# Optimization experiments

Measured on AMD Instinct MI355X. Metric: run time of the kernel, lower is better.

Reference implementation:

```python
import jax, jax.numpy as jnp
import numpy as np

H = 16  # n_heads (init kwarg)


def pos_enc(length, dim):
    # torch PositionalEncoding: pe[:,0::2]=sin, pe[:,1::2]=cos
    pos = jnp.arange(length, dtype=jnp.float32)[:, None]
    div = jnp.exp(jnp.arange(0, dim, 2, dtype=jnp.float32) * (-np.log(10000.0) / dim))
    ang = pos * div  # [L, dim/2]
    return jnp.stack([jnp.sin(ang), jnp.cos(ang)], axis=-1).reshape(length, dim)


def torch_ln(x, a, b, eps=1e-6):
    # custom LayerNorm: a*(x-mean)/(std+eps)+b with unbiased std (torch default)
    mean = x.mean(-1, keepdims=True)
    n = x.shape[-1]
    var = ((x - mean) ** 2).sum(-1, keepdims=True) / (n - 1)
    return a * (x - mean) / (jnp.sqrt(var) + eps) + b


def setup_inputs() -> dict:
    key = jax.random.key(0)
    ks = jax.random.split(key, 16)
    B, Lq, Lk, qd, kd, hid, mid = 8, 512, 1024, 768, 768, 1024, 4096
    s = 0.02  # weight init scale
    w = lambda k, shape: jax.random.normal(k, shape, jnp.float32) * s
    return dict(
        q=jax.random.normal(ks[0], (B, Lq, qd), jnp.float32),
        k=jax.random.normal(ks[1], (B, Lk, kd), jnp.float32),
        Wq=w(ks[2], (qd, hid)), bq=jnp.zeros(hid, jnp.float32),
        Wk=w(ks[3], (kd, hid)), bk=jnp.zeros(hid, jnp.float32),
        Wv=w(ks[4], (kd, hid)), bv=jnp.zeros(hid, jnp.float32),
        Wv0=w(ks[5], (kd, hid)), bv0=jnp.zeros(hid, jnp.float32),
        Wq0=w(ks[6], (qd, hid)), bq0=jnp.zeros(hid, jnp.float32),
        nq_a=jnp.ones(hid, jnp.float32), nq_b=jnp.zeros(hid, jnp.float32),
        nx_a=jnp.ones(hid, jnp.float32), nx_b=jnp.zeros(hid, jnp.float32),
        W1=w(ks[7], (hid, mid)), b1=jnp.zeros(mid, jnp.float32),
        W2=w(ks[8], (mid, hid)), b2=jnp.zeros(hid, jnp.float32),
        ns_a=jnp.ones(hid, jnp.float32), ns_b=jnp.zeros(hid, jnp.float32),
    )


def reference(q, k, Wq, bq, Wk, bk, Wv, bv, Wv0, bv0, Wq0, bq0,
              nq_a, nq_b, nx_a, nx_b, W1, b1, W2, b2, ns_a, ns_b):
    # FocalAtt(mode='CA').forward(q, k, PE='qk', SF=True, outmode='atted_bilinear')
    B, Lq, qd = q.shape
    Lk, kd = k.shape[1], k.shape[2]
    hid = Wq.shape[1]
    dh = hid // H
    q0 = q
    qp = q + pos_enc(Lq, qd)  # PosEnc_q (dropout=0)
    kp = k + pos_enc(Lk, kd)  # PosEnc_k
    # AttM: manual multi-head scores
    qh = (qp @ Wq + bq).reshape(B, Lq, H, dh).transpose(0, 2, 1, 3)  # bhqd
    kh = (kp @ Wk + bk).reshape(B, Lk, H, dh).transpose(0, 2, 1, 3)  # bhkd
    scores = jnp.einsum('bhqd,bhkd->bhqk', qh, kh) / jnp.sqrt(jnp.float32(dh))
    att = jax.nn.softmax(scores, axis=-1)  # SF=True
    q0p = q0 @ Wq0 + bq0  # [B, Lq, hid]
    # 'atted' branch
    v1 = (kp @ Wv + bv).reshape(B, Lk, H, dh).transpose(0, 2, 1, 3)
    atted = jnp.einsum('bhqk,bhkd->bhqd', att, v1)
    atted = atted.transpose(0, 2, 1, 3).reshape(B, Lq, hid)
    atted = torch_ln(q0p + atted, nq_a, nq_b)
    # 'bilinear' branch: einsum('bhvk,bhvq,bhqk->bhk')
    q0h = q0p.reshape(B, Lq, H, dh).transpose(0, 2, 1, 3)  # bhvd, v=Lq
    v0 = (kp @ Wv0 + bv0).reshape(B, Lk, H, dh).transpose(0, 2, 1, 3)  # bhqd, q=Lk
    x = jnp.einsum('bhvd,bhvq,bhqd->bhd', q0h, att, v0).reshape(B, hid)
    x = torch_ln(x, nx_a, nx_b)
    # attention output: relu over scores, mean over heads
    att_out = jax.nn.relu(scores).sum(axis=1) / jnp.float32(H)  # [B, Lq, Lk]
    # SorCA: FFN + residual + LayerNorm
    ff = jax.nn.relu(atted @ W1 + b1) @ W2 + b2
    qq = torch_ln(atted + ff, ns_a, ns_b)
    # FocalAtt returns (feature, q, k, attention, attidx_q, attidx_k); drop Nones
    return (x, qq, kp, att_out)
```

## Files before the change

kernel.cpp:

```cpp
#include <hip/hip_runtime.h>


typedef unsigned short bfr;
using short8 = __attribute__((ext_vector_type(8))) short;
using f32x4  = __attribute__((ext_vector_type(4))) float;

__device__ __forceinline__ float b2f(bfr s) {
  return __uint_as_float(((unsigned int)s) << 16);
}
__device__ __forceinline__ bfr f2b(float f) {
  unsigned int u = __float_as_uint(f);
  u += 0x7fffu + ((u >> 16) & 1u);
  return (bfr)(u >> 16);
}

struct __align__(8) us4 { bfr x, y, z, w; };

__device__ __forceinline__ float4 load4f(const float* p) { return *(const float4*)p; }
__device__ __forceinline__ float4 load4f(const bfr* p) {
  us4 u = *(const us4*)p;
  return make_float4(b2f(u.x), b2f(u.y), b2f(u.z), b2f(u.w));
}
__device__ __forceinline__ void store4(float* p, float a, float b, float c, float d) {
  *(float4*)p = make_float4(a, b, c, d);
}
__device__ __forceinline__ void store4(bfr* p, float a, float b, float c, float d) {
  us4 v; v.x = f2b(a); v.y = f2b(b); v.z = f2b(c); v.w = f2b(d);
  *(us4*)p = v;
}

__device__ __forceinline__ void gll16(const bfr* g, bfr* l) {
  __builtin_amdgcn_global_load_lds(
      (const __attribute__((address_space(1))) unsigned int*)g,
      (__attribute__((address_space(3))) unsigned int*)l, 16, 0, 0);
}

__device__ __forceinline__ int swz_off(int row, int chunk) {
  return row * 64 + ((chunk ^ (row & 7)) * 8);
}

__device__ __forceinline__ float pe_val(int l, int d) {
  float ang = (float)l * expf((float)(d & ~1) * (-9.210340371976184f / 768.0f));
  return (d & 1) ? cosf(ang) : sinf(ang);
}

__global__ __launch_bounds__(256) void posenc_k(const float* __restrict__ in,
                                                float* __restrict__ outf,
                                                bfr* __restrict__ outb, int total) {
  int idx = blockIdx.x * 256 + threadIdx.x;
  if (idx >= total) return;
  float v = in[idx] + pe_val((idx / 768) % 1024, idx % 768);
  outf[idx] = v;
  outb[idx] = f2b(v);
}

__global__ __launch_bounds__(256) void posenc_q_all(const float* __restrict__ in,
                                                    bfr* __restrict__ out,
                                                    bfr* __restrict__ outraw,
                                                    int total) {
  int idx = blockIdx.x * 256 + threadIdx.x;
  if (idx >= total) return;
  float v = in[idx];
  out[idx] = f2b(v + pe_val((idx / 768) % 512, idx % 768));
  outraw[idx] = f2b(v);
}

__global__ __launch_bounds__(256) void transpose_w(const float* __restrict__ src,
                                                   bfr* __restrict__ dst,
                                                   int rows, int cols, int ld,
                                                   int mode) {
  __shared__ float t[32][33];
  const int bc = blockIdx.x * 32, br = blockIdx.y * 32;
  const int tx = threadIdx.x & 31, ty = threadIdx.x >> 5;
#pragma unroll
  for (int i = 0; i < 4; i++)
    t[ty + i * 8][tx] = src[(size_t)(br + ty + i * 8) * ld + bc + tx];
  __syncthreads();
#pragma unroll
  for (int i = 0; i < 4; i++) {
    int c = bc + ty + i * 8;
    int r = (mode == 0) ? c : ((c >> 6) * 128 + (c & 63) + (mode == 2 ? 64 : 0));
    dst[(size_t)r * rows + br + tx] = f2b(t[tx][ty + i * 8]);
  }
}

template <typename TC>
__device__ __forceinline__ void mgemm_body64(const bfr* __restrict__ A,
                                             const bfr* __restrict__ BT,
                                             const float* __restrict__ bias,
                                             TC* __restrict__ C,
                                             int K, int ldc, int relu, int accum,
                                             int m0, int n0,
                                             bfr* __restrict__ As,
                                             bfr* __restrict__ Bs) {
  const int tid = threadIdx.x;
  const int lane = tid & 63, w = tid >> 6;
  const int wm = (w & 1) * 64, wn = (w >> 1) * 32;
  const int grow = lane >> 3;
  const int gkc = ((lane & 7) ^ (lane >> 3)) * 8;
  const int fr = lane & 15, fcg = lane >> 4;
  const int NT = K >> 6;
  f32x4 acc[4][2];
#pragma unroll
  for (int i = 0; i < 4; i++)
#pragma unroll
    for (int j = 0; j < 2; j++) acc[i][j] = (f32x4){0.f, 0.f, 0.f, 0.f};

  auto issue = [&](int t, int buf) {
    const int k0 = t << 6;
    const bfr* Ag = A + (size_t)(m0 + w * 32 + grow) * K + k0 + gkc;
#pragma unroll
    for (int i = 0; i < 4; i++)
      gll16(Ag + (size_t)(i * 8) * K, As + buf * 8192 + (w * 32 + i * 8) * 64);
    const bfr* Bg = BT + (size_t)(n0 + w * 16 + grow) * K + k0 + gkc;
#pragma unroll
    for (int i = 0; i < 2; i++)
      gll16(Bg + (size_t)(i * 8) * K, Bs + buf * 4096 + (w * 16 + i * 8) * 64);
  };

  issue(0, 0);
  asm volatile("s_waitcnt vmcnt(0)" ::: "memory");
  __builtin_amdgcn_s_barrier();
  __builtin_amdgcn_sched_barrier(0);
  int cur = 0;
  for (int t = 0; t < NT; ++t) {
    const bool more = (t + 1 < NT);
    if (more) issue(t + 1, cur ^ 1);
    __builtin_amdgcn_s_setprio(1);
#pragma unroll
    for (int ks = 0; ks < 2; ks++) {
      short8 af[4], bf4[2];
#pragma unroll
      for (int i = 0; i < 4; i++)
        af[i] = *(const short8*)(As + cur * 8192 + swz_off(wm + i * 16 + fr, ks * 4 + fcg));
#pragma unroll
      for (int j = 0; j < 2; j++)
        bf4[j] = *(const short8*)(Bs + cur * 4096 + swz_off(wn + j * 16 + fr, ks * 4 + fcg));
#pragma unroll
      for (int i = 0; i < 4; i++)
#pragma unroll
        for (int j = 0; j < 2; j++)
          acc[i][j] = __builtin_amdgcn_mfma_f32_16x16x32_bf16(af[i], bf4[j], acc[i][j], 0, 0, 0);
    }
    __builtin_amdgcn_s_setprio(0);
    if (more) {
      asm volatile("s_waitcnt vmcnt(0)" ::: "memory");
      __builtin_amdgcn_s_barrier();
      __builtin_amdgcn_sched_barrier(0);
      cur ^= 1;
    }
  }
  const int col0 = n0 + wn + fr;
  const int row0 = m0 + wm + (lane >> 4) * 4;
  float bsv[2];
#pragma unroll
  for (int j = 0; j < 2; j++) bsv[j] = bias ? bias[col0 + j * 16] : 0.f;
#pragma unroll
  for (int i = 0; i < 4; i++) {
#pragma unroll
    for (int j = 0; j < 2; j++) {
      const int col = col0 + j * 16;
#pragma unroll
      for (int r = 0; r < 4; r++) {
        const int row = row0 + i * 16 + r;
        float v = acc[i][j][r] + bsv[j];
        if (relu) v = fmaxf(v, 0.f);
        size_t idx = (size_t)row * ldc + col;
        if constexpr (sizeof(TC) == 2) {
          C[idx] = f2b(v);
        } else {
          if (accum) C[idx] += v; else C[idx] = v;
        }
      }
    }
  }
}

template <typename TC>
__global__ __launch_bounds__(256) void mgemm64(const bfr* __restrict__ A,
                                               const bfr* __restrict__ BT,
                                               const float* __restrict__ bias,
                                               TC* __restrict__ C,
                                               int K, int ldc, int relu, int accum) {
  __shared__ bfr As[2][8192];
  __shared__ bfr Bs[2][4096];
  const int nwg = gridDim.x * gridDim.y;
  const int bid = blockIdx.y * gridDim.x + blockIdx.x;
  const int q8 = nwg >> 3, r8 = nwg & 7;
  const int xcd = bid & 7, off = bid >> 3;
  const int swz = (xcd < r8 ? xcd * (q8 + 1) : r8 * (q8 + 1) + (xcd - r8) * q8) + off;
  const int n0 = (swz % gridDim.x) * 64, m0 = (swz / gridDim.x) * 128;
  mgemm_body64<TC>(A, BT, bias, C, K, ldc, relu, accum, m0, n0,
                   &As[0][0], &Bs[0][0]);
}

__global__ __launch_bounds__(256) void kv_gemm2(const bfr* __restrict__ kp0,
                                                const bfr* __restrict__ kp1,
                                                const bfr* __restrict__ WkT,
                                                const float* __restrict__ bk,
                                                bfr* __restrict__ kh0,
                                                bfr* __restrict__ kh1,
                                                const bfr* __restrict__ WTvv,
                                                bfr* __restrict__ vT0,
                                                bfr* __restrict__ vT1) {
  __shared__ bfr As[2][8192];
  __shared__ bfr Bs[2][4096];
  const int swz = (blockIdx.x & 7) * 96 + (blockIdx.x >> 3);
  if (swz < 128) {
    mgemm_body64<bfr>(kp0, WkT, bk, kh0, 768, 1024, 0, 0,
                      (swz >> 4) * 128, (swz & 15) * 64, &As[0][0], &Bs[0][0]);
  } else if (swz < 256) {
    const int s = swz - 128;
    mgemm_body64<bfr>(kp1, WkT, bk, kh1, 768, 1024, 0, 0,
                      (s >> 4) * 128, (s & 15) * 64, &As[0][0], &Bs[0][0]);
  } else if (swz < 512) {
    const int s = swz - 256;
    mgemm_body64<bfr>(WTvv, kp0, nullptr, vT0, 768, 1024, 0, 0,
                      (s >> 4) * 128, (s & 15) * 64, &As[0][0], &Bs[0][0]);
  } else {
    const int s = swz - 512;
    mgemm_body64<bfr>(WTvv, kp1, nullptr, vT1, 768, 1024, 0, 0,
                      (s >> 4) * 128, (s & 15) * 64, &As[0][0], &Bs[0][0]);
  }
}

__global__ __launch_bounds__(256) void proj_gemm(const bfr* __restrict__ q16,
                                                 const bfr* __restrict__ Wq0T,
                                                 const float* __restrict__ bq0,
                                                 bfr* __restrict__ q0p,
                                                 const bfr* __restrict__ qp_all,
                                                 const bfr* __restrict__ WqT,
                                                 const float* __restrict__ bq,
                                                 bfr* __restrict__ qh) {
  __shared__ bfr As[2][8192];
  __shared__ bfr Bs[2][4096];
  const int swz = (blockIdx.x & 7) * 128 + (blockIdx.x >> 3);
  if (swz < 512) {
    mgemm_body64<bfr>(q16, Wq0T, bq0, q0p, 768, 1024, 0, 0,
                      (swz >> 4) * 128, (swz & 15) * 64, &As[0][0], &Bs[0][0]);
  } else {
    const int s = swz - 512;
    mgemm_body64<bfr>(qp_all, WqT, bq, qh, 768, 1024, 0, 0,
                      (s >> 4) * 128, (s & 15) * 64, &As[0][0], &Bs[0][0]);
  }
}

__global__ __launch_bounds__(256) void score_mfma(const bfr* __restrict__ qh,
                                                  const bfr* __restrict__ kh,
                                                  bfr* __restrict__ sc) {
  __shared__ __align__(16) bfr Qs[128][72];
  __shared__ __align__(16) bfr Ks[128][72];
  const int h = blockIdx.z, q0 = blockIdx.y * 128, k0 = blockIdx.x * 128;
  const int tid = threadIdx.x, lane = tid & 63;
  const int wm = ((tid >> 6) & 1) * 64, wn = (tid >> 7) * 64;
  const int fr = lane & 15, fc = (lane >> 4) * 8;
  {
    const int r = tid >> 1, c = (tid & 1) * 32;
    const bfr* qsrc = qh + (size_t)(q0 + r) * 1024 + h * 64 + c;
    const bfr* ksrc = kh + (size_t)(k0 + r) * 1024 + h * 64 + c;
#pragma unroll
    for (int i = 0; i < 4; i++) {
      *(short8*)&Qs[r][c + i * 8] = *(const short8*)(qsrc + i * 8);
      *(short8*)&Ks[r][c + i * 8] = *(const short8*)(ksrc + i * 8);
    }
  }
  __syncthreads();
  f32x4 acc[4][4];
#pragma unroll
  for (int i = 0; i < 4; i++)
#pragma unroll
    for (int j = 0; j < 4; j++) acc[i][j] = (f32x4){0.f, 0.f, 0.f, 0.f};
  __builtin_amdgcn_s_setprio(1);
#pragma unroll
  for (int ks = 0; ks < 2; ks++) {
    short8 af[4], bf[4];
#pragma unroll
    for (int t = 0; t < 4; t++) af[t] = *(const short8*)&Qs[wm + t * 16 + fr][ks * 32 + fc];
#pragma unroll
    for (int t = 0; t < 4; t++) bf[t] = *(const short8*)&Ks[wn + t * 16 + fr][ks * 32 + fc];
#pragma unroll
    for (int i = 0; i < 4; i++)
#pragma unroll
      for (int j = 0; j < 4; j++)
        acc[i][j] = __builtin_amdgcn_mfma_f32_16x16x32_bf16(af[i], bf[j], acc[i][j], 0, 0, 0);
  }
  __builtin_amdgcn_s_setprio(0);
  const int col0 = k0 + wn + fr;
  const int row0 = q0 + wm + (lane >> 4) * 4;
#pragma unroll
  for (int i = 0; i < 4; i++)
#pragma unroll
    for (int j = 0; j < 4; j++)
#pragma unroll
      for (int r = 0; r < 4; r++)
        sc[((size_t)h * 512 + row0 + i * 16 + r) * 1024 + col0 + j * 16] =
            f2b(acc[i][j][r] * 0.125f);
}

__global__ __launch_bounds__(256) void attout8(const bfr* __restrict__ sc,
                                               float* __restrict__ ao) {
  const int i8 = (blockIdx.x * 256 + threadIdx.x) * 8;
  float s[8] = {};
#pragma unroll
  for (int h = 0; h < 16; h++) {
    short8 r = *(const short8*)(sc + (size_t)h * 524288 + i8);
#pragma unroll
    for (int e = 0; e < 8; e++) s[e] += fmaxf(b2f((bfr)r[e]), 0.f);
  }
  store4(ao + i8, s[0] * 0.0625f, s[1] * 0.0625f, s[2] * 0.0625f, s[3] * 0.0625f);
  store4(ao + i8 + 4, s[4] * 0.0625f, s[5] * 0.0625f, s[6] * 0.0625f, s[7] * 0.0625f);
}

__global__ __launch_bounds__(256) void attv4(const bfr* __restrict__ sc,
                                             const bfr* __restrict__ vT,
                                             const float* __restrict__ bv,
                                             const float* __restrict__ bv0,
                                             bfr* __restrict__ atp,
                                             bfr* __restrict__ u) {
  __shared__ bfr attL[16][1032];
  __shared__ bfr Bs[2][128 * 64];
  const int h = blockIdx.y, q0 = blockIdx.x * 16;
  const int tid = threadIdx.x, lane = tid & 63, w = tid >> 6;
  const int fr = lane & 15, fcg = lane >> 4;
  const int wn = w * 32;
  const bfr* vb = vT + (size_t)h * 128 * 1024;
  const int grow = lane >> 3;
  const int gkc = ((lane & 7) ^ (lane >> 3)) * 8;

  auto issueV = [&](int t, int buf) {
    const int k0 = t << 6;
#pragma unroll
    for (int i = 0; i < 4; i++)
      gll16(vb + (size_t)(wn + i * 8 + grow) * 1024 + k0 + gkc,
            &Bs[buf][(wn + i * 8) * 64]);
  };

  issueV(0, 0);

  const int row = tid >> 4, seg = tid & 15;
  const bfr* srow = sc + ((size_t)h * 512 + q0 + row) * 1024;
  short8 raw[8];
#pragma unroll
  for (int j = 0; j < 8; j++)
    raw[j] = *(const short8*)(srow + j * 128 + seg * 8);
  float v[64];
#pragma unroll
  for (int j = 0; j < 8; j++)
#pragma unroll
    for (int e = 0; e < 8; e++)
      v[j * 8 + e] = b2f((bfr)raw[j][e]);
  float m = v[0];
#pragma unroll
  for (int i = 1; i < 64; i++) m = fmaxf(m, v[i]);
#pragma unroll
  for (int o = 1; o < 16; o <<= 1) m = fmaxf(m, __shfl_xor(m, o, 64));
  float s = 0.f;
#pragma unroll
  for (int i = 0; i < 64; i++) { v[i] = expf(v[i] - m); s += v[i]; }
#pragma unroll
  for (int o = 1; o < 16; o <<= 1) s += __shfl_xor(s, o, 64);
  const float inv = 1.0f / s;
#pragma unroll
  for (int j = 0; j < 8; j++) {
    short8 pw;
#pragma unroll
    for (int e = 0; e < 8; e++) pw[e] = (short)f2b(v[j * 8 + e] * inv);
    *(short8*)&attL[row][j * 128 + seg * 8] = pw;
  }
  asm volatile("s_waitcnt vmcnt(0)" ::: "memory");
  __syncthreads();

  f32x4 acc[2];
#pragma unroll
  for (int j = 0; j < 2; j++) acc[j] = (f32x4){0.f, 0.f, 0.f, 0.f};
  int cur = 0;
  for (int t = 0; t < 16; ++t) {
    const bool more = (t + 1 < 16);
    if (more) issueV(t + 1, cur ^ 1);
    __builtin_amdgcn_s_setprio(1);
#pragma unroll
    for (int ks = 0; ks < 2; ks++) {
      short8 af = *(const short8*)&attL[fr][(t << 6) + ks * 32 + fcg * 8];
#pragma unroll
      for (int j = 0; j < 2; j++) {
        short8 bf = *(const short8*)&Bs[cur][swz_off(wn + j * 16 + fr, ks * 4 + fcg)];
        acc[j] = __builtin_amdgcn_mfma_f32_16x16x32_bf16(af, bf, acc[j], 0, 0, 0);
      }
    }
    __builtin_amdgcn_s_setprio(0);
    if (more) {
      asm volatile("s_waitcnt vmcnt(0)" ::: "memory");
      __builtin_amdgcn_s_barrier();
      __builtin_amdgcn_sched_barrier(0);
      cur ^= 1;
    }
  }
  const int row0 = q0 + (lane >> 4) * 4;
  bfr* o = (w < 2) ? atp : u;
  const float* bias = (w < 2) ? bv : bv0;
  const int dbase = wn & 63;
#pragma unroll
  for (int j = 0; j < 2; j++) {
    const int cm = dbase + j * 16 + fr;
    const float bb = bias[h * 64 + cm];
#pragma unroll
    for (int r = 0; r < 4; r++)
      o[(size_t)(row0 + r) * 1024 + h * 64 + cm] = f2b(acc[j][r] + bb);
  }
}

__global__ __launch_bounds__(256) void xpre2(const bfr* __restrict__ q0p0,
                                             const bfr* __restrict__ u0,
                                             float* __restrict__ xpre0) {
  const int c = blockIdx.x * 256 + threadIdx.x;
  const int r0 = blockIdx.y * 64;
  const int j = blockIdx.z;
  const bfr* qp = q0p0 + (size_t)j * 524288 + (size_t)r0 * 1024 + c;
  const bfr* up = u0 + (size_t)j * 1048576 + (size_t)r0 * 1024 + c;
  float s = 0.f;
#pragma unroll 8
  for (int r = 0; r < 64; r++)
    s = fmaf(b2f(qp[(size_t)r * 1024]), b2f(up[(size_t)r * 1024]), s);
  atomicAdd(&xpre0[j * 1024 + c], s);
}

template <typename OT>
__device__ __forceinline__ void ln_body(float4 v, const float* ga, const float* be,
                                        OT* outp, int tid, float* sm) {
  float s = v.x + v.y + v.z + v.w;
  for (int o = 32; o; o >>= 1) s += __shfl_down(s, o, 64);
  if ((tid & 63) == 0) sm[tid >> 6] = s;
  __syncthreads();
  s = sm[0] + sm[1] + sm[2] + sm[3];
  float mean = s * (1.0f / 1024.0f);
  float d0 = v.x - mean, d1 = v.y - mean, d2 = v.z - mean, d3 = v.w - mean;
  float q = d0 * d0 + d1 * d1 + d2 * d2 + d3 * d3;
  __syncthreads();
  for (int o = 32; o; o >>= 1) q += __shfl_down(q, o, 64);
  if ((tid & 63) == 0) sm[tid >> 6] = q;
  __syncthreads();
  q = sm[0] + sm[1] + sm[2] + sm[3];
  float rs = 1.0f / (sqrtf(q * (1.0f / 1023.0f)) + 1e-6f);
  float4 g = *(const float4*)(ga + tid * 4);
  float4 bb = *(const float4*)(be + tid * 4);
  store4(outp, g.x * d0 * rs + bb.x, g.y * d1 * rs + bb.y,
         g.z * d2 * rs + bb.z, g.w * d3 * rs + bb.w);
}

template <typename TX, typename TY, typename OT>
__global__ __launch_bounds__(256) void ln_kernel(const TX* __restrict__ X,
                                                 const TY* __restrict__ Y,
                                                 const float* __restrict__ ga,
                                                 const float* __restrict__ be,
                                                 OT* __restrict__ out) {
  __shared__ float sm[4];
  const size_t row = blockIdx.x;
  const int tid = threadIdx.x;
  float4 v = load4f(X + row * 1024 + tid * 4);
  if (Y) {
    float4 w = load4f(Y + row * 1024 + tid * 4);
    v.x += w.x; v.y += w.y; v.z += w.z; v.w += w.w;
  }
  ln_body(v, ga, be, out + row * 1024 + tid * 4, tid, sm);
}

__global__ __launch_bounds__(256) void ln2_kernel(const bfr* __restrict__ q0p0,
                                                  const bfr* __restrict__ atp0,
                                                  const float* __restrict__ ga,
                                                  const float* __restrict__ be,
                                                  bfr* __restrict__ atl0) {
  __shared__ float sm[4];
  const int row = blockIdx.x;
  const int b = row >> 9, r = row & 511;
  const int tid = threadIdx.x;
  float4 v = load4f(q0p0 + (size_t)b * 524288 + (size_t)r * 1024 + tid * 4);
  float4 w = load4f(atp0 + (size_t)b * 1048576 + (size_t)r * 1024 + tid * 4);
  v.x += w.x; v.y += w.y; v.z += w.z; v.w += w.w;
  ln_body(v, ga, be, atl0 + (size_t)b * 524288 + (size_t)r * 1024 + tid * 4, tid, sm);
}

extern "C" void kernel_launch(void* const* d_in, const int* in_sizes, int n_in,
                              void* d_out, int out_size, void* d_ws, size_t ws_size,
                              hipStream_t stream) {
  (void)in_sizes; (void)n_in; (void)out_size; (void)ws_size;
  const float* q   = (const float*)d_in[0];
  const float* k   = (const float*)d_in[1];
  const float* Wq  = (const float*)d_in[2];
  const float* bq  = (const float*)d_in[3];
  const float* Wk  = (const float*)d_in[4];
  const float* bk  = (const float*)d_in[5];
  const float* Wv  = (const float*)d_in[6];
  const float* bv  = (const float*)d_in[7];
  const float* Wv0 = (const float*)d_in[8];
  const float* bv0 = (const float*)d_in[9];
  const float* Wq0 = (const float*)d_in[10];
  const float* bq0 = (const float*)d_in[11];
  const float* nqa = (const float*)d_in[12];
  const float* nqb = (const float*)d_in[13];
  const float* nxa = (const float*)d_in[14];
  const float* nxb = (const float*)d_in[15];
  const float* W1  = (const float*)d_in[16];
  const float* b1  = (const float*)d_in[17];
  const float* W2  = (const float*)d_in[18];
  const float* b2  = (const float*)d_in[19];
  const float* nsa = (const float*)d_in[20];
  const float* nsb = (const float*)d_in[21];

  float* out = (float*)d_out;
  float* x_out  = out;
  float* qq_out = out + 8192;
  float* kp_out = out + 4202496;
  float* ao_out = out + 10493952;
  bfr* kp16 = (bfr*)qq_out;
  bfr* vT1  = kp16 + 6291456;

  char* base = (char*)d_ws;
  bfr* q0p   = (bfr*)(base + 0);
  bfr* qh    = (bfr*)(base + 8388608);
  bfr* atl   = (bfr*)(base + 16777216);
  bfr* WqT   = (bfr*)(base + 25165824);
  bfr* Wq0T  = (bfr*)(base + 26738688);
  bfr* WTkv  = (bfr*)(base + 28311552);
  float* xpre = (float*)(base + 33030144);
  char* S = base + 33062912;
  bfr* sc    = (bfr*)(S + 0);
  bfr* kh0   = (bfr*)(S + 16777216);
  bfr* kh1   = (bfr*)(S + 18874368);
  bfr* vT0   = (bfr*)(S + 20971520);
  bfr* atp0  = (bfr*)(S + 16777216);
  bfr* ub0   = (bfr*)(S + 17825792);
  bfr* atp1  = (bfr*)(S + 18874368);
  bfr* ub1   = (bfr*)(S + 19922944);
  bfr* qp_all = (bfr*)(S + 0);
  bfr* q16    = (bfr*)(S + 6291456);
  bfr* W1Tn  = (bfr*)(S + 0);
  bfr* W2Tn  = (bfr*)(S + 4194304);
  bfr* ff1n  = (bfr*)(S + 8388608);
  float* ff2a = (float*)(base + 0);

  posenc_k<<<24576, 256, 0, stream>>>(k, kp_out, kp16, 6291456);
  posenc_q_all<<<12288, 256, 0, stream>>>(q, qp_all, q16, 3145728);
  transpose_w<<<dim3(32, 24), 256, 0, stream>>>(Wq, WqT, 768, 1024, 1024, 0);
  transpose_w<<<dim3(32, 24), 256, 0, stream>>>(Wq0, Wq0T, 768, 1024, 1024, 0);
  transpose_w<<<dim3(32, 24), 256, 0, stream>>>(Wk, WTkv, 768, 1024, 1024, 0);
  transpose_w<<<dim3(32, 24), 256, 0, stream>>>(Wv, WTkv + 786432, 768, 1024, 1024, 1);
  transpose_w<<<dim3(32, 24), 256, 0, stream>>>(Wv0, WTkv + 786432, 768, 1024, 1024, 2);

  proj_gemm<<<1024, 256, 0, stream>>>(q16, Wq0T, bq0, q0p, qp_all, WqT, bq, qh);
  hipMemsetAsync(xpre, 0, 32768, stream);

  for (int p = 0; p < 4; p++) {
    const int b0 = 2 * p;
    kv_gemm2<<<768, 256, 0, stream>>>(kp16 + (size_t)b0 * 786432,
                                      kp16 + (size_t)(b0 + 1) * 786432,
                                      WTkv, bk, kh0, kh1,
                                      WTkv + 786432, vT0, vT1);
    for (int j = 0; j < 2; j++) {
      const int b = b0 + j;
      bfr* kh = j ? kh1 : kh0;
      bfr* vT = j ? vT1 : vT0;
      bfr* atpb = j ? atp1 : atp0;
      bfr* ub = j ? ub1 : ub0;
      score_mfma<<<dim3(8, 4, 16), 256, 0, stream>>>(qh + (size_t)b * 524288, kh, sc);
      attout8<<<256, 256, 0, stream>>>(sc, ao_out + (size_t)b * 524288);
      attv4<<<dim3(32, 16), 256, 0, stream>>>(sc, vT, bv, bv0, atpb, ub);
    }
    xpre2<<<dim3(4, 8, 2), 256, 0, stream>>>(q0p + (size_t)b0 * 524288, ub0,
                                             xpre + b0 * 1024);
    ln2_kernel<<<1024, 256, 0, stream>>>(q0p + (size_t)b0 * 524288, atp0,
                                         nqa, nqb, atl + (size_t)b0 * 524288);
  }

  ln_kernel<float, float, float><<<8, 256, 0, stream>>>(xpre, (const float*)nullptr,
                                                        nxa, nxb, x_out);

  for (int nc = 0; nc < 2; nc++) {
    transpose_w<<<dim3(64, 32), 256, 0, stream>>>(W1 + nc * 2048, W1Tn,
                                                  1024, 2048, 4096, 0);
    transpose_w<<<dim3(32, 64), 256, 0, stream>>>(W2 + (size_t)nc * 2048 * 1024, W2Tn,
                                                  2048, 1024, 1024, 0);
    mgemm64<bfr><<<dim3(32, 32), 256, 0, stream>>>(
        atl, W1Tn, b1 + nc * 2048, ff1n, 1024, 2048, 1, 0);
    mgemm64<float><<<dim3(16, 32), 256, 0, stream>>>(
        ff1n, W2Tn, nc == 0 ? b2 : nullptr, ff2a, 2048, 1024, 0, nc);
  }
  ln_kernel<bfr, float, float><<<4096, 256, 0, stream>>>(atl, ff2a, nsa, nsb, qq_out);
}
```

Before: 713.4 us.

## Restructure FFN into M-chunked full-width GEMMs with 128x128 tile kernel

The FFN now transposes W1 and W2 once, at full width, into the qq output buffer (later overwritten by the final layer norm). It then splits the work along rows (M) into two halves instead of along the hidden dimension. This drops the fp32 accumulate pass on the second GEMM and halves the transpose launches. A new 128x128-tile MFMA GEMM is added for the first FFN projection to get more reuse per tile. Separately, the relu-mean attention-output kernel now processes 4 elements per thread with twice as many blocks, for more parallelism.

```diff
diff --git a/kernel.cpp b/kernel.cpp
--- a/kernel.cpp
+++ b/kernel.cpp
@@ -192,6 +192,103 @@
   const int n0 = (swz % gridDim.x) * 64, m0 = (swz / gridDim.x) * 128;
   mgemm_body64<TC>(A, BT, bias, C, K, ldc, relu, accum, m0, n0,
                    &As[0][0], &Bs[0][0]);
+}
+
+template <typename TC>
+__global__ __launch_bounds__(256) void mgemm128(const bfr* __restrict__ A,
+                                                const bfr* __restrict__ BT,
+                                                const float* __restrict__ bias,
+                                                TC* __restrict__ C,
+                                                int K, int ldc, int relu, int accum) {
+  __shared__ bfr As[2][8192];
+  __shared__ bfr Bs[2][8192];
+  const int nwg = gridDim.x * gridDim.y;
+  const int bid = blockIdx.y * gridDim.x + blockIdx.x;
+  const int q8 = nwg >> 3, r8 = nwg & 7;
+  const int xcd = bid & 7, off = bid >> 3;
+  const int swz = (xcd < r8 ? xcd * (q8 + 1) : r8 * (q8 + 1) + (xcd - r8) * q8) + off;
+  const int n0 = (swz % gridDim.x) * 128, m0 = (swz / gridDim.x) * 128;
+  const int tid = threadIdx.x;
+  const int lane = tid & 63, w = tid >> 6;
+  const int wm = (w & 1) * 64, wn = (w >> 1) * 64;
+  const int grow = lane >> 3;
+  const int gkc = ((lane & 7) ^ (lane >> 3)) * 8;
+  const int fr = lane & 15, fcg = lane >> 4;
+  const int NT = K >> 6;
+  f32x4 acc[4][4];
+#pragma unroll
+  for (int i = 0; i < 4; i++)
+#pragma unroll
+    for (int j = 0; j < 4; j++) acc[i][j] = (f32x4){0.f, 0.f, 0.f, 0.f};
+
+  auto issue = [&](int t, int buf) {
+    const int k0 = t << 6;
+    const bfr* Ag = A + (size_t)(m0 + w * 32 + grow) * K + k0 + gkc;
+#pragma unroll
+    for (int i = 0; i < 4; i++)
+      gll16(Ag + (size_t)(i * 8) * K, &As[buf][(w * 32 + i * 8) * 64]);
+    const bfr* Bg = BT + (size_t)(n0 + w * 32 + grow) * K + k0 + gkc;
+#pragma unroll
+    for (int i = 0; i < 4; i++)
+      gll16(Bg + (size_t)(i * 8) * K, &Bs[buf][(w * 32 + i * 8) * 64]);
+  };
+
+  issue(0, 0);
+  asm volatile("s_waitcnt vmcnt(0)" ::: "memory");
+  __builtin_amdgcn_s_barrier();
+  __builtin_amdgcn_sched_barrier(0);
+  int cur = 0;
+  for (int t = 0; t < NT; ++t) {
+    const bool more = (t + 1 < NT);
+    if (more) issue(t + 1, cur ^ 1);
+    __builtin_amdgcn_s_setprio(1);
+#pragma unroll
+    for (int ks = 0; ks < 2; ks++) {
+      short8 af[4], bf4[4];
+#pragma unroll
+      for (int i = 0; i < 4; i++)
+        af[i] = *(const short8*)&As[cur][swz_off(wm + i * 16 + fr, ks * 4 + fcg)];
+#pragma unroll
+      for (int j = 0; j < 4; j++)
+        bf4[j] = *(const short8*)&Bs[cur][swz_off(wn + j * 16 + fr, ks * 4 + fcg)];
+#pragma unroll
+      for (int i = 0; i < 4; i++)
+#pragma unroll
+        for (int j = 0; j < 4; j++)
+          acc[i][j] = __builtin_amdgcn_mfma_f32_16x16x32_bf16(af[i], bf4[j], acc[i][j], 0, 0, 0);
+    }
+    __builtin_amdgcn_s_setprio(0);
+    if (more) {
+      asm volatile("s_waitcnt vmcnt(0)" ::: "memory");
+      __builtin_amdgcn_s_barrier();
+      __builtin_amdgcn_sched_barrier(0);
+      cur ^= 1;
+    }
+  }
+  const int col0 = n0 + wn + fr;
+  const int row0 = m0 + wm + (lane >> 4) * 4;
+  float bsv[4];
+#pragma unroll
+  for (int j = 0; j < 4; j++) bsv[j] = bias ? bias[col0 + j * 16] : 0.f;
+#pragma unroll
+  for (int i = 0; i < 4; i++) {
+#pragma unroll
+    for (int j = 0; j < 4; j++) {
+      const int col = col0 + j * 16;
+#pragma unroll
+      for (int r = 0; r < 4; r++) {
+        const int row = row0 + i * 16 + r;
+        float v = acc[i][j][r] + bsv[j];
+        if (relu) v = fmaxf(v, 0.f);
+        size_t idx = (size_t)row * ldc + col;
+        if constexpr (sizeof(TC) == 2) {
+          C[idx] = f2b(v);
+        } else {
+          if (accum) C[idx] += v; else C[idx] = v;
+        }
+      }
+    }
+  }
 }
 
 __global__ __launch_bounds__(256) void kv_gemm2(const bfr* __restrict__ kp0,
@@ -297,18 +394,17 @@
             f2b(acc[i][j][r] * 0.125f);
 }
 
-__global__ __launch_bounds__(256) void attout8(const bfr* __restrict__ sc,
+__global__ __launch_bounds__(256) void attout4(const bfr* __restrict__ sc,
                                                float* __restrict__ ao) {
-  const int i8 = (blockIdx.x * 256 + threadIdx.x) * 8;
-  float s[8] = {};
+  const int i4 = (blockIdx.x * 256 + threadIdx.x) * 4;
+  float s[4] = {};
 #pragma unroll
   for (int h = 0; h < 16; h++) {
-    short8 r = *(const short8*)(sc + (size_t)h * 524288 + i8);
-#pragma unroll
-    for (int e = 0; e < 8; e++) s[e] += fmaxf(b2f((bfr)r[e]), 0.f);
-  }
-  store4(ao + i8, s[0] * 0.0625f, s[1] * 0.0625f, s[2] * 0.0625f, s[3] * 0.0625f);
-  store4(ao + i8 + 4, s[4] * 0.0625f, s[5] * 0.0625f, s[6] * 0.0625f, s[7] * 0.0625f);
+    us4 r = *(const us4*)(sc + (size_t)h * 524288 + i4);
+    s[0] += fmaxf(b2f(r.x), 0.f); s[1] += fmaxf(b2f(r.y), 0.f);
+    s[2] += fmaxf(b2f(r.z), 0.f); s[3] += fmaxf(b2f(r.w), 0.f);
+  }
+  store4(ao + i4, s[0] * 0.0625f, s[1] * 0.0625f, s[2] * 0.0625f, s[3] * 0.0625f);
 }
 
 __global__ __launch_bounds__(256) void attv4(const bfr* __restrict__ sc,
@@ -513,6 +609,8 @@
   float* ao_out = out + 10493952;
   bfr* kp16 = (bfr*)qq_out;
   bfr* vT1  = kp16 + 6291456;
+  bfr* W1Tf = (bfr*)qq_out;
+  bfr* W2Tf = W1Tf + 4194304;
 
   char* base = (char*)d_ws;
   bfr* q0p   = (bfr*)(base + 0);
@@ -533,9 +631,7 @@
   bfr* ub1   = (bfr*)(S + 19922944);
   bfr* qp_all = (bfr*)(S + 0);
   bfr* q16    = (bfr*)(S + 6291456);
-  bfr* W1Tn  = (bfr*)(S + 0);
-  bfr* W2Tn  = (bfr*)(S + 4194304);
-  bfr* ff1n  = (bfr*)(S + 8388608);
+  bfr* ff1n  = (bfr*)(S + 0);
   float* ff2a = (float*)(base + 0);
 
   posenc_k<<<24576, 256, 0, stream>>>(k, kp_out, kp16, 6291456);
@@ -562,7 +658,7 @@
       bfr* atpb = j ? atp1 : atp0;
       bfr* ub = j ? ub1 : ub0;
       score_mfma<<<dim3(8, 4, 16), 256, 0, stream>>>(qh + (size_t)b * 524288, kh, sc);
-      attout8<<<256, 256, 0, stream>>>(sc, ao_out + (size_t)b * 524288);
+      attout4<<<512, 256, 0, stream>>>(sc, ao_out + (size_t)b * 524288);
       attv4<<<dim3(32, 16), 256, 0, stream>>>(sc, vT, bv, bv0, atpb, ub);
     }
     xpre2<<<dim3(4, 8, 2), 256, 0, stream>>>(q0p + (size_t)b0 * 524288, ub0,
@@ -574,15 +670,13 @@
   ln_kernel<float, float, float><<<8, 256, 0, stream>>>(xpre, (const float*)nullptr,
                                                         nxa, nxb, x_out);
 
-  for (int nc = 0; nc < 2; nc++) {
-    transpose_w<<<dim3(64, 32), 256, 0, stream>>>(W1 + nc * 2048, W1Tn,
-                                                  1024, 2048, 4096, 0);
-    transpose_w<<<dim3(32, 64), 256, 0, stream>>>(W2 + (size_t)nc * 2048 * 1024, W2Tn,
-                                                  2048, 1024, 1024, 0);
-    mgemm64<bfr><<<dim3(32, 32), 256, 0, stream>>>(
-        atl, W1Tn, b1 + nc * 2048, ff1n, 1024, 2048, 1, 0);
-    mgemm64<float><<<dim3(16, 32), 256, 0, stream>>>(
-        ff1n, W2Tn, nc == 0 ? b2 : nullptr, ff2a, 2048, 1024, 0, nc);
+  transpose_w<<<dim3(128, 32), 256, 0, stream>>>(W1, W1Tf, 1024, 4096, 4096, 0);
+  transpose_w<<<dim3(32, 128), 256, 0, stream>>>(W2, W2Tf, 4096, 1024, 1024, 0);
+  for (int mc = 0; mc < 2; mc++) {
+    mgemm128<bfr><<<dim3(32, 16), 256, 0, stream>>>(
+        atl + (size_t)mc * 2097152, W1Tf, b1, ff1n, 1024, 4096, 1, 0);
+    mgemm64<float><<<dim3(16, 16), 256, 0, stream>>>(
+        ff1n, W2Tf, b2, ff2a + (size_t)mc * 2097152, 4096, 1024, 0, 0);
   }
   ln_kernel<bfr, float, float><<<4096, 256, 0, stream>>>(atl, ff2a, nsa, nsb, qq_out);
 }
```

New measurement: 713.9 us. No clear change (+0.1%).
